# Performance work log

Measured on AMD Instinct MI355X. Metric: run time of the kernel, lower is better.

Reference implementation:

```python
import jax, jax.numpy as jnp
import numpy as np

VOCAB = 32000
DIM = 512
FFN = 4 * DIM
LAYERS_PER_BLOCK = [2, 2, 2]
THRESHOLDS = [3.5e-05, 4.0e-05, 1.0]
N_LAYERS = sum(LAYERS_PER_BLOCK)
B, S = 4, 1024


def setup_inputs() -> dict:
    key = jax.random.key(0)
    ks = jax.random.split(key, 8)
    x = jax.random.randint(ks[0], (B, S), 0, VOCAB)
    emb = jax.random.normal(ks[1], (VOCAB, DIM), jnp.float32) * 0.02
    head = jax.random.normal(ks[2], (VOCAB, DIM), jnp.float32) * (1.0 / np.sqrt(DIM))
    Wv = jax.random.normal(ks[3], (N_LAYERS, DIM, DIM), jnp.float32) * 0.02
    Wo = jax.random.normal(ks[4], (N_LAYERS, DIM, DIM), jnp.float32) * 0.02
    W1 = jax.random.normal(ks[5], (N_LAYERS, DIM, FFN), jnp.float32) * 0.02
    W2 = jax.random.normal(ks[6], (N_LAYERS, FFN, DIM), jnp.float32) * 0.02
    ln1_s = jnp.ones((N_LAYERS, DIM), jnp.float32)
    ln1_b = jnp.zeros((N_LAYERS, DIM), jnp.float32)
    ln2_s = jnp.ones((N_LAYERS, DIM), jnp.float32)
    ln2_b = jnp.zeros((N_LAYERS, DIM), jnp.float32)
    return {"x": x, "emb": emb, "head": head, "Wv": Wv, "Wo": Wo,
            "W1": W1, "W2": W2, "ln1_s": ln1_s, "ln1_b": ln1_b,
            "ln2_s": ln2_s, "ln2_b": ln2_b}


def _ln(x, s, b):
    m = jnp.mean(x, axis=-1, keepdims=True)
    v = jnp.mean((x - m) ** 2, axis=-1, keepdims=True)
    return (x - m) * jax.lax.rsqrt(v + 1e-5) * s + b


def reference(x, emb, head, Wv, Wo, W1, W2, ln1_s, ln1_b, ln2_s, ln2_b):
    T = B * S
    h = emb[x.reshape(-1)]                      # (T, dim) embedding gather
    active = jnp.ones((T,), dtype=bool)
    final_logits = jnp.zeros((T, VOCAB), jnp.float32)
    layer = 0
    n_blocks = len(LAYERS_PER_BLOCK)
    for b_idx, (n_l, thr) in enumerate(zip(LAYERS_PER_BLOCK, THRESHOLDS)):
        hb = h
        for l in range(layer, layer + n_l):
            # seq_len==1 attention: softmax over single key == 1 -> out = V @ Wo
            hn = _ln(hb, ln1_s[l], ln1_b[l])
            hb = hb + (hn @ Wv[l]) @ Wo[l]
            hn2 = _ln(hb, ln2_s[l], ln2_b[l])
            hb = hb + jax.nn.gelu(hn2 @ W1[l]) @ W2[l]
        layer += n_l
        logits = hb @ head.T                    # (T, vocab)
        conf = jnp.max(jax.nn.softmax(logits, axis=-1), axis=-1)
        is_last = b_idx == n_blocks - 1
        should_exit = conf > thr
        exit_now = active & (should_exit | is_last)   # scatter exiting tokens
        final_logits = jnp.where(exit_now[:, None], logits, final_logits)
        cont = active & ~exit_now
        h = jnp.where(cont[:, None], hb, h)           # only continuing tokens updated
        active = cont
    return final_logits.reshape(B, S, VOCAB)
```

## Files before the change

### kernel.cpp

```cpp
#include <hip/hip_runtime.h>
#include <hip/hip_bf16.h>
#include <math.h>

#define TT 4096
#define DIM 512
#define FFN 2048
#define NVOCAB 32000
#define NGRP 500

typedef __attribute__((ext_vector_type(8))) short short8_t;
typedef __attribute__((ext_vector_type(4))) float f32x4;

__device__ __forceinline__ float gelu_f(float x) {
    float x3 = x * x * x;
    float u = 0.7978845608028654f * (x + 0.044715f * x3);
    return 0.5f * x * (1.0f + tanhf(u));
}

__device__ __forceinline__ unsigned short f2bf_rn(float f) {
    unsigned u = __float_as_uint(f);
    u += 0x7FFFu + ((u >> 16) & 1u);
    return (unsigned short)(u >> 16);
}

__global__ __launch_bounds__(128) void gather_kernel(const int* __restrict__ x,
                                                     const float* __restrict__ emb,
                                                     float* __restrict__ h,
                                                     int* __restrict__ flags) {
    int t = blockIdx.x;
    int idx = x[t];
    const float4 v = *(const float4*)&emb[(size_t)idx * DIM + threadIdx.x * 4];
    *(float4*)&h[(size_t)t * DIM + threadIdx.x * 4] = v;
    if (threadIdx.x == 0) flags[t] = 1;
}

__global__ __launch_bounds__(256) void cvt_hilo(const float* __restrict__ src,
                                                short* __restrict__ hi,
                                                short* __restrict__ lo, int n4) {
    int i = blockIdx.x * 256 + threadIdx.x;
    if (i >= n4) return;
    float4 v = *(const float4*)&src[(size_t)i * 4];
    float f[4] = {v.x, v.y, v.z, v.w};
    short4 hv, lv;
    short* hp = &hv.x;
    short* lp = &lv.x;
#pragma unroll
    for (int j = 0; j < 4; ++j) {
        unsigned short hb = f2bf_rn(f[j]);
        float hf = __uint_as_float((unsigned)hb << 16);
        unsigned short lb = f2bf_rn(f[j] - hf);
        hp[j] = (short)hb;
        lp[j] = (short)lb;
    }
    *(short4*)&hi[(size_t)i * 4] = hv;
    *(short4*)&lo[(size_t)i * 4] = lv;
}

__global__ __launch_bounds__(256) void cvt_bf16(const float* __restrict__ src,
                                                short* __restrict__ hi, int n4) {
    int i = blockIdx.x * 256 + threadIdx.x;
    if (i >= n4) return;
    float4 v = *(const float4*)&src[(size_t)i * 4];
    float f[4] = {v.x, v.y, v.z, v.w};
    short4 hv;
    short* hp = &hv.x;
#pragma unroll
    for (int j = 0; j < 4; ++j) hp[j] = (short)f2bf_rn(f[j]);
    *(short4*)&hi[(size_t)i * 4] = hv;
}

__global__ __launch_bounds__(256) void cvt_w_t(const float* __restrict__ W,
                                               short* __restrict__ hiT,
                                               short* __restrict__ loT,
                                               int K, int N) {
    __shared__ short hs[32][36];
    __shared__ short ls[32][36];
    const int n0 = blockIdx.x * 32, k0 = blockIdx.y * 32;
    const int r = threadIdx.x >> 3, c4 = (threadIdx.x & 7) << 2;
    float4 v = *(const float4*)&W[(size_t)(k0 + r) * N + n0 + c4];
    float f[4] = {v.x, v.y, v.z, v.w};
#pragma unroll
    for (int j = 0; j < 4; ++j) {
        unsigned short hb = f2bf_rn(f[j]);
        float hf = __uint_as_float((unsigned)hb << 16);
        unsigned short lb = f2bf_rn(f[j] - hf);
        hs[r][c4 + j] = (short)hb;
        ls[r][c4 + j] = (short)lb;
    }
    __syncthreads();
    const int nr = threadIdx.x >> 3, kc4 = (threadIdx.x & 7) << 2;
    short4 hv, lv;
    short* hp = &hv.x;
    short* lp = &lv.x;
#pragma unroll
    for (int j = 0; j < 4; ++j) {
        hp[j] = hs[kc4 + j][nr];
        lp[j] = ls[kc4 + j][nr];
    }
    *(short4*)&hiT[(size_t)(n0 + nr) * K + k0 + kc4] = hv;
    *(short4*)&loT[(size_t)(n0 + nr) * K + k0 + kc4] = lv;
}

__global__ __launch_bounds__(256) void cvt_w_t_hi(const float* __restrict__ W,
                                                  short* __restrict__ hiT,
                                                  int K, int N) {
    __shared__ short hs[32][36];
    const int n0 = blockIdx.x * 32, k0 = blockIdx.y * 32;
    const int r = threadIdx.x >> 3, c4 = (threadIdx.x & 7) << 2;
    float4 v = *(const float4*)&W[(size_t)(k0 + r) * N + n0 + c4];
    float f[4] = {v.x, v.y, v.z, v.w};
#pragma unroll
    for (int j = 0; j < 4; ++j) hs[r][c4 + j] = (short)f2bf_rn(f[j]);
    __syncthreads();
    const int nr = threadIdx.x >> 3, kc4 = (threadIdx.x & 7) << 2;
    short4 hv;
    short* hp = &hv.x;
#pragma unroll
    for (int j = 0; j < 4; ++j) hp[j] = hs[kc4 + j][nr];
    *(short4*)&hiT[(size_t)(n0 + nr) * K + k0 + kc4] = hv;
}

template<bool IDX>
__global__ __launch_bounds__(256) void ln_kernel(const float* __restrict__ x,
                                                 const float* __restrict__ gam,
                                                 const float* __restrict__ bet,
                                                 float* __restrict__ out,
                                                 const int* __restrict__ idx,
                                                 const int* __restrict__ cnt) {
    int wv = threadIdx.x >> 6, lane = threadIdx.x & 63;
    int p = (blockIdx.x << 2) | wv;
    if (IDX && p >= *cnt) return;
    int t = IDX ? idx[p] : p;
    const float* row = x + (size_t)t * DIM;
    int base = lane * 8;
    float4 v0 = *(const float4*)&row[base];
    float4 v1 = *(const float4*)&row[base + 4];
    float s = v0.x + v0.y + v0.z + v0.w + v1.x + v1.y + v1.z + v1.w;
#pragma unroll
    for (int o = 32; o; o >>= 1) s += __shfl_xor(s, o, 64);
    float mean = s * (1.0f / (float)DIM);
    float d0 = v0.x - mean, d1 = v0.y - mean, d2 = v0.z - mean, d3 = v0.w - mean;
    float d4 = v1.x - mean, d5 = v1.y - mean, d6 = v1.z - mean, d7 = v1.w - mean;
    float q = d0*d0 + d1*d1 + d2*d2 + d3*d3 + d4*d4 + d5*d5 + d6*d6 + d7*d7;
#pragma unroll
    for (int o = 32; o; o >>= 1) q += __shfl_xor(q, o, 64);
    float var = q * (1.0f / (float)DIM);
    float rs = 1.0f / sqrtf(var + 1e-5f);
    float4 g0 = *(const float4*)&gam[base];
    float4 g1 = *(const float4*)&gam[base + 4];
    float4 b0 = *(const float4*)&bet[base];
    float4 b1 = *(const float4*)&bet[base + 4];
    float4 o0, o1;
    o0.x = d0 * rs * g0.x + b0.x;  o0.y = d1 * rs * g0.y + b0.y;
    o0.z = d2 * rs * g0.z + b0.z;  o0.w = d3 * rs * g0.w + b0.w;
    o1.x = d4 * rs * g1.x + b1.x;  o1.y = d5 * rs * g1.y + b1.y;
    o1.z = d6 * rs * g1.z + b1.z;  o1.w = d7 * rs * g1.w + b1.w;
    float* orow = out + (size_t)p * DIM;
    *(float4*)&orow[base] = o0;
    *(float4*)&orow[base + 4] = o1;
}

__global__ __launch_bounds__(256) void ln_hilo(const float* __restrict__ x,
                                               const float* __restrict__ gam,
                                               const float* __restrict__ bet,
                                               short* __restrict__ ohi,
                                               short* __restrict__ olo) {
    int wv = threadIdx.x >> 6, lane = threadIdx.x & 63;
    int t = (blockIdx.x << 2) | wv;
    const float* row = x + (size_t)t * DIM;
    int base = lane * 8;
    float4 v0 = *(const float4*)&row[base];
    float4 v1 = *(const float4*)&row[base + 4];
    float s = v0.x + v0.y + v0.z + v0.w + v1.x + v1.y + v1.z + v1.w;
#pragma unroll
    for (int o = 32; o; o >>= 1) s += __shfl_xor(s, o, 64);
    float mean = s * (1.0f / (float)DIM);
    float d[8] = {v0.x - mean, v0.y - mean, v0.z - mean, v0.w - mean,
                  v1.x - mean, v1.y - mean, v1.z - mean, v1.w - mean};
    float q = 0.0f;
#pragma unroll
    for (int j = 0; j < 8; ++j) q += d[j] * d[j];
#pragma unroll
    for (int o = 32; o; o >>= 1) q += __shfl_xor(q, o, 64);
    float var = q * (1.0f / (float)DIM);
    float rs = 1.0f / sqrtf(var + 1e-5f);
    float g[8], bb[8];
    *(float4*)&g[0] = *(const float4*)&gam[base];
    *(float4*)&g[4] = *(const float4*)&gam[base + 4];
    *(float4*)&bb[0] = *(const float4*)&bet[base];
    *(float4*)&bb[4] = *(const float4*)&bet[base + 4];
    short8_t hv, lv;
#pragma unroll
    for (int j = 0; j < 8; ++j) {
        float val = d[j] * rs * g[j] + bb[j];
        unsigned short hb = f2bf_rn(val);
        float hf = __uint_as_float((unsigned)hb << 16);
        hv[j] = (short)hb;
        lv[j] = (short)f2bf_rn(val - hf);
    }
    *(short8_t*)&ohi[(size_t)t * DIM + base] = hv;
    *(short8_t*)&olo[(size_t)t * DIM + base] = lv;
}

__device__ __forceinline__ void epi_store(int EPI, float val, size_t off,
                                          float* Cf, short* oHi, short* oLo) {
    if (EPI == 3) {
        Cf[off] = val;
    } else if (EPI == 2) {
        Cf[off] += val;
    } else if (EPI == 4) {
        float nv = Cf[off] + val;
        Cf[off] = nv;
        unsigned short hb = f2bf_rn(nv);
        float hf = __uint_as_float((unsigned)hb << 16);
        oHi[off] = (short)hb;
        oLo[off] = (short)f2bf_rn(nv - hf);
    } else {
        if (EPI == 1) val = gelu_f(val);
        unsigned short hb = f2bf_rn(val);
        float hf = __uint_as_float((unsigned)hb << 16);
        oHi[off] = (short)hb;
        oLo[off] = (short)f2bf_rn(val - hf);
    }
}

template<int EPI>
__global__ __launch_bounds__(256) void gemm_l_mfma(const short* __restrict__ Ah,
                                                   const short* __restrict__ Al,
                                                   const short* __restrict__ Bh,
                                                   const short* __restrict__ Bl,
                                                   float* __restrict__ Cf,
                                                   short* __restrict__ oHi,
                                                   short* __restrict__ oLo,
                                                   int N, int K) {
    __shared__ __align__(16) short sm[16384];
    short* sAh = sm;
    short* sAl = sm + 4096;
    short* sBh = sm + 8192;
    short* sBl = sm + 12288;
    const int tid = threadIdx.x;
    const int wv = tid >> 6, lane = tid & 63;
    const int m0 = blockIdx.x * 128;
    const int n0 = blockIdx.y * 128;
    const int wm = (wv & 1) * 64, wn = (wv >> 1) * 64;
    const int r16 = lane >> 2;
    const int gsw = ((lane & 3) ^ (r16 & 3)) << 3;
    const int fr = lane & 15;
    const int q = lane >> 4;

    f32x4 acc[4][4];
#pragma unroll
    for (int i = 0; i < 4; ++i)
#pragma unroll
        for (int j = 0; j < 4; ++j)
            acc[i][j] = (f32x4){0.0f, 0.0f, 0.0f, 0.0f};

    const int NKT = K >> 5;
    for (int kt = 0; kt < NKT; ++kt) {
        const int k0 = kt << 5;
        __syncthreads();
#pragma unroll
        for (int j = 0; j < 2; ++j) {
            const int rr = (wv << 5) + (j << 4);
            const int gr = rr + r16;
            const short* ga_h = Ah + (size_t)(m0 + gr) * K + k0 + gsw;
            const short* ga_l = Al + (size_t)(m0 + gr) * K + k0 + gsw;
            const short* gb_h = Bh + (size_t)(n0 + gr) * K + k0 + gsw;
            const short* gb_l = Bl + (size_t)(n0 + gr) * K + k0 + gsw;
            __builtin_amdgcn_global_load_lds((const __attribute__((address_space(1))) void*)ga_h,
                                             (__attribute__((address_space(3))) void*)(sAh + rr * 32), 16, 0, 0);
            __builtin_amdgcn_global_load_lds((const __attribute__((address_space(1))) void*)ga_l,
                                             (__attribute__((address_space(3))) void*)(sAl + rr * 32), 16, 0, 0);
            __builtin_amdgcn_global_load_lds((const __attribute__((address_space(1))) void*)gb_h,
                                             (__attribute__((address_space(3))) void*)(sBh + rr * 32), 16, 0, 0);
            __builtin_amdgcn_global_load_lds((const __attribute__((address_space(1))) void*)gb_l,
                                             (__attribute__((address_space(3))) void*)(sBl + rr * 32), 16, 0, 0);
        }
        __syncthreads();
        short8_t ah[4], al[4], bh[4], bl[4];
#pragma unroll
        for (int i = 0; i < 4; ++i) {
            const int ra = wm + i * 16 + fr;
            const int rb = wn + i * 16 + fr;
            const int swa = (q ^ (fr & 3)) << 3;
            ah[i] = *(const short8_t*)&sAh[ra * 32 + swa];
            al[i] = *(const short8_t*)&sAl[ra * 32 + swa];
            bh[i] = *(const short8_t*)&sBh[rb * 32 + swa];
            bl[i] = *(const short8_t*)&sBl[rb * 32 + swa];
        }
#pragma unroll
        for (int i = 0; i < 4; ++i)
#pragma unroll
            for (int j = 0; j < 4; ++j) {
                acc[i][j] = __builtin_amdgcn_mfma_f32_16x16x32_bf16(ah[i], bh[j], acc[i][j], 0, 0, 0);
                acc[i][j] = __builtin_amdgcn_mfma_f32_16x16x32_bf16(ah[i], bl[j], acc[i][j], 0, 0, 0);
                acc[i][j] = __builtin_amdgcn_mfma_f32_16x16x32_bf16(al[i], bh[j], acc[i][j], 0, 0, 0);
            }
    }
    const int row_base = (lane >> 4) << 2;
#pragma unroll
    for (int i = 0; i < 4; ++i)
#pragma unroll
        for (int j = 0; j < 4; ++j) {
            const int row = m0 + wm + i * 16 + row_base;
            const int col = n0 + wn + j * 16 + fr;
#pragma unroll
            for (int r = 0; r < 4; ++r)
                epi_store(EPI, acc[i][j][r], (size_t)(row + r) * N + col, Cf, oHi, oLo);
        }
}

template<int EPI>
__global__ __launch_bounds__(256) void gemm_l2(const short* __restrict__ Ah,
                                               const short* __restrict__ Al,
                                               const short* __restrict__ Bh,
                                               float* __restrict__ Cf,
                                               short* __restrict__ oHi,
                                               short* __restrict__ oLo,
                                               int N, int K) {
    __shared__ __align__(16) short sm[12288];
    short* sAh = sm;
    short* sAl = sm + 4096;
    short* sBh = sm + 8192;
    const int tid = threadIdx.x;
    const int wv = tid >> 6, lane = tid & 63;
    const int m0 = blockIdx.x * 128;
    const int n0 = blockIdx.y * 128;
    const int wm = (wv & 1) * 64, wn = (wv >> 1) * 64;
    const int r16 = lane >> 2;
    const int gsw = ((lane & 3) ^ (r16 & 3)) << 3;
    const int fr = lane & 15;
    const int q = lane >> 4;

    f32x4 acc[4][4];
#pragma unroll
    for (int i = 0; i < 4; ++i)
#pragma unroll
        for (int j = 0; j < 4; ++j)
            acc[i][j] = (f32x4){0.0f, 0.0f, 0.0f, 0.0f};

    const int NKT = K >> 5;
    for (int kt = 0; kt < NKT; ++kt) {
        const int k0 = kt << 5;
        __syncthreads();
#pragma unroll
        for (int j = 0; j < 2; ++j) {
            const int rr = (wv << 5) + (j << 4);
            const int gr = rr + r16;
            const short* ga_h = Ah + (size_t)(m0 + gr) * K + k0 + gsw;
            const short* ga_l = Al + (size_t)(m0 + gr) * K + k0 + gsw;
            const short* gb_h = Bh + (size_t)(n0 + gr) * K + k0 + gsw;
            __builtin_amdgcn_global_load_lds((const __attribute__((address_space(1))) void*)ga_h,
                                             (__attribute__((address_space(3))) void*)(sAh + rr * 32), 16, 0, 0);
            __builtin_amdgcn_global_load_lds((const __attribute__((address_space(1))) void*)ga_l,
                                             (__attribute__((address_space(3))) void*)(sAl + rr * 32), 16, 0, 0);
            __builtin_amdgcn_global_load_lds((const __attribute__((address_space(1))) void*)gb_h,
                                             (__attribute__((address_space(3))) void*)(sBh + rr * 32), 16, 0, 0);
        }
        __syncthreads();
        short8_t ah[4], al[4], bh[4];
#pragma unroll
        for (int i = 0; i < 4; ++i) {
            const int ra = wm + i * 16 + fr;
            const int rb = wn + i * 16 + fr;
            const int swa = (q ^ (fr & 3)) << 3;
            ah[i] = *(const short8_t*)&sAh[ra * 32 + swa];
            al[i] = *(const short8_t*)&sAl[ra * 32 + swa];
            bh[i] = *(const short8_t*)&sBh[rb * 32 + swa];
        }
#pragma unroll
        for (int i = 0; i < 4; ++i)
#pragma unroll
            for (int j = 0; j < 4; ++j) {
                acc[i][j] = __builtin_amdgcn_mfma_f32_16x16x32_bf16(ah[i], bh[j], acc[i][j], 0, 0, 0);
                acc[i][j] = __builtin_amdgcn_mfma_f32_16x16x32_bf16(al[i], bh[j], acc[i][j], 0, 0, 0);
            }
    }
    const int row_base = (lane >> 4) << 2;
#pragma unroll
    for (int i = 0; i < 4; ++i)
#pragma unroll
        for (int j = 0; j < 4; ++j) {
            const int row = m0 + wm + i * 16 + row_base;
            const int col = n0 + wn + j * 16 + fr;
#pragma unroll
            for (int r = 0; r < 4; ++r)
                epi_store(EPI, acc[i][j][r], (size_t)(row + r) * N + col, Cf, oHi, oLo);
        }
}

template<int EPI>
__global__ __launch_bounds__(256) void gemm_l64b(const short* __restrict__ Ah,
                                                 const short* __restrict__ Al,
                                                 const short* __restrict__ Bh,
                                                 float* __restrict__ Cf,
                                                 short* __restrict__ oHi,
                                                 short* __restrict__ oLo,
                                                 int N, int K) {
    __shared__ __align__(16) short sm[8192];
    short* sAh = sm;
    short* sAl = sm + 2048;
    short* sBh = sm + 4096;
    const int tid = threadIdx.x;
    const int wv = tid >> 6, lane = tid & 63;
    const int m0 = blockIdx.x * 64;
    const int n0 = blockIdx.y * 128;
    const int wm = (wv & 1) * 32, wn = (wv >> 1) * 64;
    const int r16 = lane >> 2;
    const int gsw = ((lane & 3) ^ (r16 & 3)) << 3;
    const int fr = lane & 15;
    const int q = lane >> 4;

    f32x4 acc[2][4];
#pragma unroll
    for (int i = 0; i < 2; ++i)
#pragma unroll
        for (int j = 0; j < 4; ++j)
            acc[i][j] = (f32x4){0.0f, 0.0f, 0.0f, 0.0f};

    const int NKT = K >> 5;
    for (int kt = 0; kt < NKT; ++kt) {
        const int k0 = kt << 5;
        __syncthreads();
        {
            const int rr = wv << 4;
            const int gr = rr + r16;
            const short* ga_h = Ah + (size_t)(m0 + gr) * K + k0 + gsw;
            const short* ga_l = Al + (size_t)(m0 + gr) * K + k0 + gsw;
            __builtin_amdgcn_global_load_lds((const __attribute__((address_space(1))) void*)ga_h,
                                             (__attribute__((address_space(3))) void*)(sAh + rr * 32), 16, 0, 0);
            __builtin_amdgcn_global_load_lds((const __attribute__((address_space(1))) void*)ga_l,
                                             (__attribute__((address_space(3))) void*)(sAl + rr * 32), 16, 0, 0);
        }
#pragma unroll
        for (int j = 0; j < 2; ++j) {
            const int rr = (wv << 5) + (j << 4);
            const int gr = rr + r16;
            const short* gb_h = Bh + (size_t)(n0 + gr) * K + k0 + gsw;
            __builtin_amdgcn_global_load_lds((const __attribute__((address_space(1))) void*)gb_h,
                                             (__attribute__((address_space(3))) void*)(sBh + rr * 32), 16, 0, 0);
        }
        __syncthreads();
        short8_t ah[2], al[2], bh[4];
        const int swa = (q ^ (fr & 3)) << 3;
#pragma unroll
        for (int i = 0; i < 2; ++i) {
            const int ra = wm + i * 16 + fr;
            ah[i] = *(const short8_t*)&sAh[ra * 32 + swa];
            al[i] = *(const short8_t*)&sAl[ra * 32 + swa];
        }
#pragma unroll
        for (int j = 0; j < 4; ++j) {
            const int rb = wn + j * 16 + fr;
            bh[j] = *(const short8_t*)&sBh[rb * 32 + swa];
        }
#pragma unroll
        for (int i = 0; i < 2; ++i)
#pragma unroll
            for (int j = 0; j < 4; ++j) {
                acc[i][j] = __builtin_amdgcn_mfma_f32_16x16x32_bf16(ah[i], bh[j], acc[i][j], 0, 0, 0);
                acc[i][j] = __builtin_amdgcn_mfma_f32_16x16x32_bf16(al[i], bh[j], acc[i][j], 0, 0, 0);
            }
    }
    const int row_base = (lane >> 4) << 2;
#pragma unroll
    for (int i = 0; i < 2; ++i)
#pragma unroll
        for (int j = 0; j < 4; ++j) {
            const int row = m0 + wm + i * 16 + row_base;
            const int col = n0 + wn + j * 16 + fr;
#pragma unroll
            for (int r = 0; r < 4; ++r)
                epi_store(EPI, acc[i][j][r], (size_t)(row + r) * N + col, Cf, oHi, oLo);
        }
}

template<int EPI>
__global__ __launch_bounds__(256) void gemm_l64(const short* __restrict__ Ah,
                                                const short* __restrict__ Al,
                                                const short* __restrict__ Bh,
                                                const short* __restrict__ Bl,
                                                float* __restrict__ Cf,
                                                short* __restrict__ oHi,
                                                short* __restrict__ oLo,
                                                int N, int K) {
    __shared__ __align__(16) short sm[12288];
    short* sAh = sm;
    short* sAl = sm + 2048;
    short* sBh = sm + 4096;
    short* sBl = sm + 8192;
    const int tid = threadIdx.x;
    const int wv = tid >> 6, lane = tid & 63;
    const int m0 = blockIdx.x * 64;
    const int n0 = blockIdx.y * 128;
    const int wm = (wv & 1) * 32, wn = (wv >> 1) * 64;
    const int r16 = lane >> 2;
    const int gsw = ((lane & 3) ^ (r16 & 3)) << 3;
    const int fr = lane & 15;
    const int q = lane >> 4;

    f32x4 acc[2][4];
#pragma unroll
    for (int i = 0; i < 2; ++i)
#pragma unroll
        for (int j = 0; j < 4; ++j)
            acc[i][j] = (f32x4){0.0f, 0.0f, 0.0f, 0.0f};

    const int NKT = K >> 5;
    for (int kt = 0; kt < NKT; ++kt) {
        const int k0 = kt << 5;
        __syncthreads();
        {
            const int rr = wv << 4;
            const int gr = rr + r16;
            const short* ga_h = Ah + (size_t)(m0 + gr) * K + k0 + gsw;
            const short* ga_l = Al + (size_t)(m0 + gr) * K + k0 + gsw;
            __builtin_amdgcn_global_load_lds((const __attribute__((address_space(1))) void*)ga_h,
                                             (__attribute__((address_space(3))) void*)(sAh + rr * 32), 16, 0, 0);
            __builtin_amdgcn_global_load_lds((const __attribute__((address_space(1))) void*)ga_l,
                                             (__attribute__((address_space(3))) void*)(sAl + rr * 32), 16, 0, 0);
        }
#pragma unroll
        for (int j = 0; j < 2; ++j) {
            const int rr = (wv << 5) + (j << 4);
            const int gr = rr + r16;
            const short* gb_h = Bh + (size_t)(n0 + gr) * K + k0 + gsw;
            const short* gb_l = Bl + (size_t)(n0 + gr) * K + k0 + gsw;
            __builtin_amdgcn_global_load_lds((const __attribute__((address_space(1))) void*)gb_h,
                                             (__attribute__((address_space(3))) void*)(sBh + rr * 32), 16, 0, 0);
            __builtin_amdgcn_global_load_lds((const __attribute__((address_space(1))) void*)gb_l,
                                             (__attribute__((address_space(3))) void*)(sBl + rr * 32), 16, 0, 0);
        }
        __syncthreads();
        short8_t ah[2], al[2], bh[4], bl[4];
        const int swa = (q ^ (fr & 3)) << 3;
#pragma unroll
        for (int i = 0; i < 2; ++i) {
            const int ra = wm + i * 16 + fr;
            ah[i] = *(const short8_t*)&sAh[ra * 32 + swa];
            al[i] = *(const short8_t*)&sAl[ra * 32 + swa];
        }
#pragma unroll
        for (int j = 0; j < 4; ++j) {
            const int rb = wn + j * 16 + fr;
            bh[j] = *(const short8_t*)&sBh[rb * 32 + swa];
            bl[j] = *(const short8_t*)&sBl[rb * 32 + swa];
        }
#pragma unroll
        for (int i = 0; i < 2; ++i)
#pragma unroll
            for (int j = 0; j < 4; ++j) {
                acc[i][j] = __builtin_amdgcn_mfma_f32_16x16x32_bf16(ah[i], bh[j], acc[i][j], 0, 0, 0);
                acc[i][j] = __builtin_amdgcn_mfma_f32_16x16x32_bf16(ah[i], bl[j], acc[i][j], 0, 0, 0);
                acc[i][j] = __builtin_amdgcn_mfma_f32_16x16x32_bf16(al[i], bh[j], acc[i][j], 0, 0, 0);
            }
    }
    const int row_base = (lane >> 4) << 2;
#pragma unroll
    for (int i = 0; i < 2; ++i)
#pragma unroll
        for (int j = 0; j < 4; ++j) {
            const int row = m0 + wm + i * 16 + row_base;
            const int col = n0 + wn + j * 16 + fr;
#pragma unroll
            for (int r = 0; r < 4; ++r)
                epi_store(EPI, acc[i][j][r], (size_t)(row + r) * N + col, Cf, oHi, oLo);
        }
}

__global__ __launch_bounds__(256) void gemm_head_bf16(const short* __restrict__ Ah,
                                                      const short* __restrict__ Bh,
                                                      float* __restrict__ C,
                                                      float2* __restrict__ pp,
                                                      int N, int K) {
    __shared__ __align__(16) short sm[8192];
    short* sA = sm;
    short* sB = sm + 4096;
    const int tid = threadIdx.x;
    const int wv = tid >> 6, lane = tid & 63;
    const int m0 = blockIdx.x * 128;
    const int n0 = blockIdx.y * 128;
    const int nt = blockIdx.y;
    const int wm = (wv & 1) * 64, wn = (wv >> 1) * 64;
    const int r16 = lane >> 2;
    const int gsw = ((lane & 3) ^ (r16 & 3)) << 3;
    const int fr = lane & 15;
    const int q = lane >> 4;

    f32x4 acc[4][4];
#pragma unroll
    for (int i = 0; i < 4; ++i)
#pragma unroll
        for (int j = 0; j < 4; ++j)
            acc[i][j] = (f32x4){0.0f, 0.0f, 0.0f, 0.0f};

    const int NKT = K >> 5;
    for (int kt = 0; kt < NKT; ++kt) {
        const int k0 = kt << 5;
        __syncthreads();
#pragma unroll
        for (int j = 0; j < 2; ++j) {
            const int rr = (wv << 5) + (j << 4);
            const int gr = rr + r16;
            const short* ga = Ah + (size_t)(m0 + gr) * K + k0 + gsw;
            const short* gb = Bh + (size_t)(n0 + gr) * K + k0 + gsw;
            __builtin_amdgcn_global_load_lds((const __attribute__((address_space(1))) void*)ga,
                                             (__attribute__((address_space(3))) void*)(sA + rr * 32), 16, 0, 0);
            __builtin_amdgcn_global_load_lds((const __attribute__((address_space(1))) void*)gb,
                                             (__attribute__((address_space(3))) void*)(sB + rr * 32), 16, 0, 0);
        }
        __syncthreads();
        short8_t ah[4], bh[4];
        const int swa = (q ^ (fr & 3)) << 3;
#pragma unroll
        for (int i = 0; i < 4; ++i) {
            ah[i] = *(const short8_t*)&sA[(wm + i * 16 + fr) * 32 + swa];
            bh[i] = *(const short8_t*)&sB[(wn + i * 16 + fr) * 32 + swa];
        }
#pragma unroll
        for (int i = 0; i < 4; ++i)
#pragma unroll
            for (int j = 0; j < 4; ++j)
                acc[i][j] = __builtin_amdgcn_mfma_f32_16x16x32_bf16(ah[i], bh[j], acc[i][j], 0, 0, 0);
    }
    const int hi = lane >> 4;
    const int row_base = hi << 2;
#pragma unroll
    for (int i = 0; i < 4; ++i)
#pragma unroll
        for (int r = 0; r < 4; ++r) {
            float v0 = acc[i][0][r], v1 = acc[i][1][r];
            float v2 = acc[i][2][r], v3 = acc[i][3][r];
            float mg = fmaxf(fmaxf(v0, v1), fmaxf(v2, v3));
#pragma unroll
            for (int o = 1; o < 16; o <<= 1) mg = fmaxf(mg, __shfl_xor(mg, o, 64));
            float sg = __expf(v0 - mg) + __expf(v1 - mg) + __expf(v2 - mg) + __expf(v3 - mg);
#pragma unroll
            for (int o = 1; o < 16; o <<= 1) sg += __shfl_xor(sg, o, 64);
            if (fr == 0)
                pp[(size_t)(m0 + wm + i * 16 + hi * 4 + r) * NGRP + nt * 2 + (wn >> 6)] =
                    make_float2(mg, sg);
        }
#pragma unroll
    for (int i = 0; i < 4; ++i)
#pragma unroll
        for (int j = 0; j < 4; ++j) {
            const int row = m0 + wm + i * 16 + row_base;
            const int col = n0 + wn + j * 16 + fr;
#pragma unroll
            for (int r = 0; r < 4; ++r)
                C[(size_t)(row + r) * N + col] = acc[i][j][r];
        }
}

__global__ __launch_bounds__(256) void conf_reduce(const float2* __restrict__ pp,
                                                   int* __restrict__ flags, float thr) {
    int wv = threadIdx.x >> 6, lane = threadIdx.x & 63;
    int t = blockIdx.x * 4 + wv;
    float m = -INFINITY, s = 0.0f;
    for (int k = lane; k < NGRP; k += 64) {
        float2 v = pp[(size_t)t * NGRP + k];
        float mm = fmaxf(m, v.x);
        s = s * __expf(m - mm) + v.y * __expf(v.x - mm);
        m = mm;
    }
#pragma unroll
    for (int o = 1; o < 64; o <<= 1) {
        float mo = __shfl_xor(m, o, 64);
        float so = __shfl_xor(s, o, 64);
        float mm = fmaxf(m, mo);
        s = s * __expf(m - mm) + so * __expf(mo - mm);
        m = mm;
    }
    if (lane == 0) {
        float conf = 1.0f / s;
        if (conf > thr) flags[t] = 0;
    }
}

template<bool ADD, bool GELU>
__global__ __launch_bounds__(256) void gemm_nn(const float* __restrict__ A,
                                               const float* __restrict__ B,
                                               float* __restrict__ C,
                                               int M, int N, int K) {
    const int m0 = blockIdx.y * 64, n0 = blockIdx.x * 64;
    __shared__ float As[16][68];
    __shared__ float Bs[16][68];
    const int tid = threadIdx.x;
    const int am = tid >> 2, ak = (tid & 3) << 2;
    const int bk = tid >> 4, bn = (tid & 15) << 2;
    const int tn = tid & 15, tm = tid >> 4;
    float acc[4][4] = {};
    for (int k0 = 0; k0 < K; k0 += 16) {
        float4 a4 = *(const float4*)&A[(size_t)(m0 + am) * K + k0 + ak];
        float4 b4 = *(const float4*)&B[(size_t)(k0 + bk) * N + n0 + bn];
        __syncthreads();
        As[ak + 0][am] = a4.x;
        As[ak + 1][am] = a4.y;
        As[ak + 2][am] = a4.z;
        As[ak + 3][am] = a4.w;
        *(float4*)&Bs[bk][bn] = b4;
        __syncthreads();
#pragma unroll
        for (int kk = 0; kk < 16; ++kk) {
            float4 av = *(const float4*)&As[kk][tm << 2];
            float4 bv = *(const float4*)&Bs[kk][tn << 2];
            float a[4] = {av.x, av.y, av.z, av.w};
            float b[4] = {bv.x, bv.y, bv.z, bv.w};
#pragma unroll
            for (int i = 0; i < 4; ++i)
#pragma unroll
                for (int j = 0; j < 4; ++j)
                    acc[i][j] = fmaf(a[i], b[j], acc[i][j]);
        }
    }
#pragma unroll
    for (int i = 0; i < 4; ++i) {
        size_t row = (size_t)(m0 + (tm << 2) + i);
        float* cp = &C[row * (size_t)N + n0 + (tn << 2)];
        float rr[4] = {acc[i][0], acc[i][1], acc[i][2], acc[i][3]};
        if (GELU) {
#pragma unroll
            for (int j = 0; j < 4; ++j) rr[j] = gelu_f(rr[j]);
        }
        if (ADD) {
            float4 cc = *(const float4*)cp;
            rr[0] += cc.x; rr[1] += cc.y; rr[2] += cc.z; rr[3] += cc.w;
        }
        float4 rv = {rr[0], rr[1], rr[2], rr[3]};
        *(float4*)cp = rv;
    }
}

template<bool ADD, bool GELU, bool SCAT>
__global__ __launch_bounds__(256) void gemm_nn_gs(const float* __restrict__ A,
                                                  const float* __restrict__ B,
                                                  float* __restrict__ C,
                                                  int N, int K,
                                                  const int* __restrict__ idx,
                                                  const int* __restrict__ cnt) {
    const int c = *cnt;
    const int ntm = (c + 63) >> 6;
    const int ntn = N >> 6;
    const int total = ntm * ntn;
    __shared__ float As[16][68];
    __shared__ float Bs[16][68];
    const int tid = threadIdx.x;
    const int am = tid >> 2, ak = (tid & 3) << 2;
    const int bk = tid >> 4, bn = (tid & 15) << 2;
    const int tn = tid & 15, tm = tid >> 4;
    for (int tile = blockIdx.x; tile < total; tile += gridDim.x) {
        const int m0 = (tile % ntm) << 6, n0 = (tile / ntm) << 6;
        int ar = m0 + am;
        ar = ar < c ? ar : c - 1;
        float acc[4][4] = {};
        for (int k0 = 0; k0 < K; k0 += 16) {
            float4 a4 = *(const float4*)&A[(size_t)ar * K + k0 + ak];
            float4 b4 = *(const float4*)&B[(size_t)(k0 + bk) * N + n0 + bn];
            __syncthreads();
            As[ak + 0][am] = a4.x;
            As[ak + 1][am] = a4.y;
            As[ak + 2][am] = a4.z;
            As[ak + 3][am] = a4.w;
            *(float4*)&Bs[bk][bn] = b4;
            __syncthreads();
#pragma unroll
            for (int kk = 0; kk < 16; ++kk) {
                float4 av = *(const float4*)&As[kk][tm << 2];
                float4 bv = *(const float4*)&Bs[kk][tn << 2];
                float a[4] = {av.x, av.y, av.z, av.w};
                float b[4] = {bv.x, bv.y, bv.z, bv.w};
#pragma unroll
                for (int i = 0; i < 4; ++i)
#pragma unroll
                    for (int j = 0; j < 4; ++j)
                        acc[i][j] = fmaf(a[i], b[j], acc[i][j]);
            }
        }
#pragma unroll
        for (int i = 0; i < 4; ++i) {
            int p = m0 + (tm << 2) + i;
            if (p >= c) continue;
            int r = SCAT ? idx[p] : p;
            float* cp = &C[(size_t)r * N + n0 + (tn << 2)];
            float rr[4] = {acc[i][0], acc[i][1], acc[i][2], acc[i][3]};
            if (GELU) {
#pragma unroll
                for (int j = 0; j < 4; ++j) rr[j] = gelu_f(rr[j]);
            }
            if (ADD) {
                float4 cc = *(const float4*)cp;
                rr[0] += cc.x; rr[1] += cc.y; rr[2] += cc.z; rr[3] += cc.w;
            }
            float4 rv = {rr[0], rr[1], rr[2], rr[3]};
            *(float4*)cp = rv;
        }
        __syncthreads();
    }
}

__global__ __launch_bounds__(256) void gemm_nt_head_gs(const float* __restrict__ A,
                                                       const float* __restrict__ Bt,
                                                       float* __restrict__ C,
                                                       const int* __restrict__ idx,
                                                       const int* __restrict__ cnt) {
    const int c = *cnt;
    const int ntm = (c + 63) >> 6;
    const int ntn = NVOCAB >> 6;
    const int total = ntm * ntn;
    __shared__ float As[16][68];
    __shared__ float Bs[16][68];
    const int tid = threadIdx.x;
    const int am = tid >> 2, ak = (tid & 3) << 2;
    const int tn = tid & 15, tm = tid >> 4;
    for (int tile = blockIdx.x; tile < total; tile += gridDim.x) {
        const int m0 = (tile % ntm) << 6, n0 = (tile / ntm) << 6;
        int ap = m0 + am;
        int ar = idx[ap < c ? ap : c - 1];
        float acc[4][4] = {};
        for (int k0 = 0; k0 < DIM; k0 += 16) {
            float4 a4 = *(const float4*)&A[(size_t)ar * DIM + k0 + ak];
            float4 b4 = *(const float4*)&Bt[(size_t)(n0 + am) * DIM + k0 + ak];
            __syncthreads();
            As[ak + 0][am] = a4.x;
            As[ak + 1][am] = a4.y;
            As[ak + 2][am] = a4.z;
            As[ak + 3][am] = a4.w;
            Bs[ak + 0][am] = b4.x;
            Bs[ak + 1][am] = b4.y;
            Bs[ak + 2][am] = b4.z;
            Bs[ak + 3][am] = b4.w;
            __syncthreads();
#pragma unroll
            for (int kk = 0; kk < 16; ++kk) {
                float4 av = *(const float4*)&As[kk][tm << 2];
                float4 bv = *(const float4*)&Bs[kk][tn << 2];
                float a[4] = {av.x, av.y, av.z, av.w};
                float b[4] = {bv.x, bv.y, bv.z, bv.w};
#pragma unroll
                for (int i = 0; i < 4; ++i)
#pragma unroll
                    for (int j = 0; j < 4; ++j)
                        acc[i][j] = fmaf(a[i], b[j], acc[i][j]);
            }
        }
#pragma unroll
        for (int i = 0; i < 4; ++i) {
            int p = m0 + (tm << 2) + i;
            if (p >= c) continue;
            int r = idx[p];
            float4 rv = {acc[i][0], acc[i][1], acc[i][2], acc[i][3]};
            *(float4*)&C[(size_t)r * NVOCAB + n0 + (tn << 2)] = rv;
        }
        __syncthreads();
    }
}

template<bool IDX>
__global__ __launch_bounds__(256) void conf_exit(const float* __restrict__ out,
                                                 int* __restrict__ flags,
                                                 const int* __restrict__ idx,
                                                 const int* __restrict__ cnt,
                                                 float thr) {
    int t;
    if (IDX) {
        if (blockIdx.x >= *cnt) return;
        t = idx[blockIdx.x];
    } else {
        t = blockIdx.x;
        if (flags[t] == 0) return;
    }
    const float4* row = (const float4*)(out + (size_t)t * NVOCAB);
    float m = -INFINITY, s = 0.0f;
    for (int i = threadIdx.x; i < NVOCAB / 4; i += 256) {
        float4 v = row[i];
        float m4 = fmaxf(fmaxf(v.x, v.y), fmaxf(v.z, v.w));
        float s4 = __expf(v.x - m4) + __expf(v.y - m4) + __expf(v.z - m4) + __expf(v.w - m4);
        if (m4 > m) {
            s = s * __expf(m - m4) + s4;
            m = m4;
        } else {
            s += s4 * __expf(m4 - m);
        }
    }
    __shared__ float ms[256], ss[256];
    ms[threadIdx.x] = m;
    ss[threadIdx.x] = s;
    __syncthreads();
    for (int st = 128; st; st >>= 1) {
        if (threadIdx.x < st) {
            float m1 = ms[threadIdx.x], s1 = ss[threadIdx.x];
            float m2 = ms[threadIdx.x + st], s2 = ss[threadIdx.x + st];
            float mm = fmaxf(m1, m2);
            ss[threadIdx.x] = s1 * __expf(m1 - mm) + s2 * __expf(m2 - mm);
            ms[threadIdx.x] = mm;
        }
        __syncthreads();
    }
    if (threadIdx.x == 0) {
        float conf = 1.0f / ss[0];
        if (conf > thr) flags[t] = 0;
    }
}

__global__ __launch_bounds__(256) void compact_kernel(const int* __restrict__ flags,
                                                      int* __restrict__ idx,
                                                      int* __restrict__ cnt) {
    __shared__ int wsum[4];
    __shared__ int base;
    if (threadIdx.x == 0) base = 0;
    int lane = threadIdx.x & 63, wv = threadIdx.x >> 6;
    for (int chunk = 0; chunk < TT; chunk += 256) {
        __syncthreads();
        int t = chunk + threadIdx.x;
        int f = flags[t];
        unsigned long long b = __ballot(f != 0);
        if (lane == 0) wsum[wv] = __popcll(b);
        __syncthreads();
        int off = base;
        for (int w = 0; w < wv; ++w) off += wsum[w];
        off += __popcll(b & ((1ull << lane) - 1));
        if (f) idx[off] = t;
        __syncthreads();
        if (threadIdx.x == 0) base += wsum[0] + wsum[1] + wsum[2] + wsum[3];
    }
    __syncthreads();
    if (threadIdx.x == 0) *cnt = base;
}

extern "C" void kernel_launch(void* const* d_in, const int* in_sizes, int n_in,
                              void* d_out, int out_size, void* d_ws, size_t ws_size,
                              hipStream_t stream) {
    const int* x = (const int*)d_in[0];
    const float* emb = (const float*)d_in[1];
    const float* head = (const float*)d_in[2];
    const float* Wv = (const float*)d_in[3];
    const float* Wo = (const float*)d_in[4];
    const float* W1 = (const float*)d_in[5];
    const float* W2 = (const float*)d_in[6];
    const float* ln1s = (const float*)d_in[7];
    const float* ln1b = (const float*)d_in[8];
    const float* ln2s = (const float*)d_in[9];
    const float* ln2b = (const float*)d_in[10];
    float* out = (float*)d_out;
    float* ws = (float*)d_ws;

    float* h  = ws;
    float* hn = ws + 2097152;
    float* tA = ws + 4194304;
    float* tF = ws + 6291456;
    short* hnHi = (short*)hn;
    short* hnLo = hnHi + TT * DIM;
    short* tAHi = (short*)tA;
    short* tALo = tAHi + TT * DIM;
    short* tFHi = (short*)tF;
    short* tFLo = tFHi + TT * FFN;
    float2* pp = (float2*)tF;
    int* flags = (int*)(ws + 14680064);
    int* idxl  = flags + TT;
    int* cntp  = flags + 2 * TT;
    short* hHi    = (short*)(ws + 14700000);
    short* hLo    = (short*)(ws + 15748576);
    short* headHi = (short*)(ws + 16797152);
    short* headLo = (short*)(ws + 24989152);
    short* wT     = (short*)(ws + 33181152);
    const size_t LSTRIDE = 5242880;
    const size_t NEED_T2 = (size_t)33181152 * 4;
    const size_t NEED_T1 = (size_t)38424032 * 4;
    const int tier = ws_size >= NEED_T1 ? 1 : (ws_size >= NEED_T2 ? 2 : 3);

    gather_kernel<<<TT, 128, 0, stream>>>(x, emb, h, flags);

    const float THR[3] = {3.5e-05f, 4.0e-05f, 1.0f};
    const dim3 gDD(DIM / 64, TT / 64), gDF(FFN / 64, TT / 64), gHead(NVOCAB / 64, TT / 64);

    if (tier == 1) {
        for (int l = 0; l < 2; ++l) {
            short* wb = wT + (size_t)l * LSTRIDE;
            cvt_hilo<<<(DIM * DIM / 4 + 255) / 256, 256, 0, stream>>>(Wv + (size_t)l * DIM * DIM, tAHi, tALo, DIM * DIM / 4);
            cvt_w_t<<<dim3(DIM / 32, DIM / 32), 256, 0, stream>>>(Wo + (size_t)l * DIM * DIM, wb + 524288, wb + 786432, DIM, DIM);
            gemm_l64<0><<<dim3(DIM / 64, DIM / 128), 256, 0, stream>>>(
                wb + 524288, wb + 786432, tAHi, tALo, nullptr, wb, wb + 262144, DIM, DIM);
            cvt_w_t_hi<<<dim3(FFN / 32, DIM / 32), 256, 0, stream>>>(W1 + (size_t)l * DIM * FFN, wb + 1048576, DIM, FFN);
            cvt_w_t_hi<<<dim3(DIM / 32, FFN / 32), 256, 0, stream>>>(W2 + (size_t)l * FFN * DIM, wb + 3145728, FFN, DIM);
        }
        for (int l = 0; l < 2; ++l) {
            short* wb = wT + (size_t)l * LSTRIDE;
            ln_hilo<<<TT / 4, 256, 0, stream>>>(h, ln1s + l * DIM, ln1b + l * DIM, hnHi, hnLo);
            gemm_l64b<2><<<dim3(TT / 64, DIM / 128), 256, 0, stream>>>(hnHi, hnLo, wb, h, nullptr, nullptr, DIM, DIM);
            ln_hilo<<<TT / 4, 256, 0, stream>>>(h, ln2s + l * DIM, ln2b + l * DIM, hnHi, hnLo);
            gemm_l2<1><<<dim3(TT / 128, FFN / 128), 256, 0, stream>>>(hnHi, hnLo, wb + 1048576, nullptr, tFHi, tFLo, FFN, DIM);
            if (l == 1) {
                gemm_l64b<4><<<dim3(TT / 64, DIM / 128), 256, 0, stream>>>(tFHi, tFLo, wb + 3145728, h, hHi, hLo, DIM, FFN);
            } else {
                gemm_l64b<2><<<dim3(TT / 64, DIM / 128), 256, 0, stream>>>(tFHi, tFLo, wb + 3145728, h, nullptr, nullptr, DIM, FFN);
            }
        }
        cvt_bf16<<<(NVOCAB * DIM / 4 + 255) / 256, 256, 0, stream>>>(head, headHi, NVOCAB * DIM / 4);
        gemm_head_bf16<<<dim3(TT / 128, NVOCAB / 128), 256, 0, stream>>>(hHi, headHi, out, pp, NVOCAB, DIM);
        conf_reduce<<<TT / 4, 256, 0, stream>>>(pp, flags, THR[0]);
    } else {
        for (int l = 0; l < 2; ++l) {
            ln_kernel<false><<<TT / 4, 256, 0, stream>>>(h, ln1s + l * DIM, ln1b + l * DIM, hn, nullptr, nullptr);
            gemm_nn<false, false><<<gDD, 256, 0, stream>>>(hn, Wv + (size_t)l * DIM * DIM, tA, TT, DIM, DIM);
            gemm_nn<true, false><<<gDD, 256, 0, stream>>>(tA, Wo + (size_t)l * DIM * DIM, h, TT, DIM, DIM);
            ln_kernel<false><<<TT / 4, 256, 0, stream>>>(h, ln2s + l * DIM, ln2b + l * DIM, hn, nullptr, nullptr);
            gemm_nn<false, true><<<gDF, 256, 0, stream>>>(hn, W1 + (size_t)l * DIM * FFN, tF, TT, FFN, DIM);
            gemm_nn<true, false><<<gDD, 256, 0, stream>>>(tF, W2 + (size_t)l * FFN * DIM, h, TT, DIM, FFN);
        }
        if (tier == 2) {
            cvt_hilo<<<(TT * DIM / 4 + 255) / 256, 256, 0, stream>>>(h, hHi, hLo, TT * DIM / 4);
            cvt_hilo<<<(NVOCAB * DIM / 4 + 255) / 256, 256, 0, stream>>>(head, headHi, headLo, NVOCAB * DIM / 4);
            gemm_l_mfma<3><<<dim3(TT / 128, NVOCAB / 128), 256, 0, stream>>>(hHi, hLo, headHi, headLo, out, nullptr, nullptr, NVOCAB, DIM);
        } else {
            compact_kernel<<<1, 256, 0, stream>>>(flags, idxl, cntp);
            gemm_nt_head_gs<<<512, 256, 0, stream>>>(h, head, out, idxl, cntp);
        }
        conf_exit<false><<<TT, 256, 0, stream>>>(out, flags, nullptr, nullptr, THR[0]);
    }
    compact_kernel<<<1, 256, 0, stream>>>(flags, idxl, cntp);

    for (int b = 1; b < 3; ++b) {
        for (int li = 0; li < 2; ++li) {
            int l = b * 2 + li;
            ln_kernel<true><<<TT / 4, 256, 0, stream>>>(h, ln1s + l * DIM, ln1b + l * DIM, hn, idxl, cntp);
            gemm_nn_gs<false, false, false><<<256, 256, 0, stream>>>(hn, Wv + (size_t)l * DIM * DIM, tA, DIM, DIM, idxl, cntp);
            gemm_nn_gs<true, false, true><<<256, 256, 0, stream>>>(tA, Wo + (size_t)l * DIM * DIM, h, DIM, DIM, idxl, cntp);
            ln_kernel<true><<<TT / 4, 256, 0, stream>>>(h, ln2s + l * DIM, ln2b + l * DIM, hn, idxl, cntp);
            gemm_nn_gs<false, true, false><<<256, 256, 0, stream>>>(hn, W1 + (size_t)l * DIM * FFN, tF, FFN, DIM, idxl, cntp);
            gemm_nn_gs<true, false, true><<<256, 256, 0, stream>>>(tF, W2 + (size_t)l * FFN * DIM, h, DIM, FFN, idxl, cntp);
        }
        gemm_nt_head_gs<<<512, 256, 0, stream>>>(h, head, out, idxl, cntp);
        if (b == 1) {
            conf_exit<true><<<TT, 256, 0, stream>>>(out, flags, idxl, cntp, THR[1]);
            compact_kernel<<<1, 256, 0, stream>>>(flags, idxl, cntp);
        }
    }
}
```

Baseline: 686.7 us.

## Double-buffer LDS in head GEMM with async global-to-LDS prefetch two stages ahead

The vocab head GEMM kernel now keeps two LDS buffers and issues direct global-to-LDS loads for tile t+2 while computing tile t. It uses explicit vmcnt waits, barriers and setprio around the MFMA block. The goal is to hide global memory latency that the old load-sync-compute loop exposed on every K step. In exchange it doubles LDS use to 32KB per block, which may lower occupancy, and adds hand-placed wait counts that must match the number of outstanding loads.

```diff
diff --git a/kernel.cpp b/kernel.cpp
--- a/kernel.cpp
+++ b/kernel.cpp
@@ -573,9 +573,7 @@
                                                       float* __restrict__ C,
                                                       float2* __restrict__ pp,
                                                       int N, int K) {
-    __shared__ __align__(16) short sm[8192];
-    short* sA = sm;
-    short* sB = sm + 4096;
+    __shared__ __align__(16) short sm[16384];
     const int tid = threadIdx.x;
     const int wv = tid >> 6, lane = tid & 63;
     const int m0 = blockIdx.x * 128;
@@ -587,6 +585,26 @@
     const int fr = lane & 15;
     const int q = lane >> 4;
 
+#define STG_HEAD(bufi, kt)                                                                \
+    {                                                                                     \
+        const int k0s = (kt) << 5;                                                        \
+        _Pragma("unroll")                                                                 \
+        for (int j = 0; j < 2; ++j) {                                                     \
+            const int rr = (wv << 5) + (j << 4);                                          \
+            const int gr = rr + r16;                                                      \
+            const short* ga = Ah + (size_t)(m0 + gr) * K + k0s + gsw;                     \
+            const short* gb = Bh + (size_t)(n0 + gr) * K + k0s + gsw;                     \
+            __builtin_amdgcn_global_load_lds(                                             \
+                (const __attribute__((address_space(1))) void*)ga,                        \
+                (__attribute__((address_space(3))) void*)(sm + (bufi) * 8192 + rr * 32),  \
+                16, 0, 0);                                                                \
+            __builtin_amdgcn_global_load_lds(                                             \
+                (const __attribute__((address_space(1))) void*)gb,                        \
+                (__attribute__((address_space(3))) void*)(sm + (bufi) * 8192 + 4096 + rr * 32), \
+                16, 0, 0);                                                                \
+        }                                                                                 \
+    }
+
     f32x4 acc[4][4];
 #pragma unroll
     for (int i = 0; i < 4; ++i)
@@ -595,34 +613,43 @@
             acc[i][j] = (f32x4){0.0f, 0.0f, 0.0f, 0.0f};
 
     const int NKT = K >> 5;
-    for (int kt = 0; kt < NKT; ++kt) {
-        const int k0 = kt << 5;
-        __syncthreads();
-#pragma unroll
-        for (int j = 0; j < 2; ++j) {
-            const int rr = (wv << 5) + (j << 4);
-            const int gr = rr + r16;
-            const short* ga = Ah + (size_t)(m0 + gr) * K + k0 + gsw;
-            const short* gb = Bh + (size_t)(n0 + gr) * K + k0 + gsw;
-            __builtin_amdgcn_global_load_lds((const __attribute__((address_space(1))) void*)ga,
-                                             (__attribute__((address_space(3))) void*)(sA + rr * 32), 16, 0, 0);
-            __builtin_amdgcn_global_load_lds((const __attribute__((address_space(1))) void*)gb,
-                                             (__attribute__((address_space(3))) void*)(sB + rr * 32), 16, 0, 0);
-        }
-        __syncthreads();
+    STG_HEAD(0, 0)
+    STG_HEAD(1, 1)
+
+    for (int t = 0; t < NKT; ++t) {
+        if (t < NKT - 1) {
+            asm volatile("s_waitcnt vmcnt(4)" ::: "memory");
+        } else {
+            asm volatile("s_waitcnt vmcnt(0)" ::: "memory");
+        }
+        __builtin_amdgcn_sched_barrier(0);
+        __builtin_amdgcn_s_barrier();
+        const int buf = t & 1;
+        const short* pA = sm + buf * 8192;
+        const short* pB = pA + 4096;
+        __builtin_amdgcn_s_setprio(1);
         short8_t ah[4], bh[4];
         const int swa = (q ^ (fr & 3)) << 3;
 #pragma unroll
         for (int i = 0; i < 4; ++i) {
-            ah[i] = *(const short8_t*)&sA[(wm + i * 16 + fr) * 32 + swa];
-            bh[i] = *(const short8_t*)&sB[(wn + i * 16 + fr) * 32 + swa];
+            ah[i] = *(const short8_t*)&pA[(wm + i * 16 + fr) * 32 + swa];
+            bh[i] = *(const short8_t*)&pB[(wn + i * 16 + fr) * 32 + swa];
         }
 #pragma unroll
         for (int i = 0; i < 4; ++i)
 #pragma unroll
             for (int j = 0; j < 4; ++j)
                 acc[i][j] = __builtin_amdgcn_mfma_f32_16x16x32_bf16(ah[i], bh[j], acc[i][j], 0, 0, 0);
-    }
+        __builtin_amdgcn_s_setprio(0);
+        asm volatile("s_waitcnt lgkmcnt(0)" ::: "memory");
+        __builtin_amdgcn_sched_barrier(0);
+        __builtin_amdgcn_s_barrier();
+        if (t + 2 < NKT) {
+            STG_HEAD(buf, t + 2)
+        }
+    }
+#undef STG_HEAD
+
     const int hi = lane >> 4;
     const int row_base = hi << 2;
 #pragma unroll
```

Measured after the change: 659.4 us. -4.0%, faster.
